# Kernel optimization log

Hardware: AMD Instinct MI355X
Metric: run time of the kernel (lower is better)

## Reference

```python
import jax, jax.numpy as jnp
import numpy as np

HEADS = 16
HEAD_DIM = 64
NEG = 1000000000.0  # additive mask magnitude from source


def setup_inputs() -> dict:
    key = jax.random.key(0)
    ks = jax.random.split(key, 6)
    N, S, D = 4, 2048, 1024
    x = jax.random.normal(ks[0], (N, S, D), dtype=jnp.float32)
    scale = 1.0 / np.sqrt(D)
    wq = jax.random.normal(ks[1], (D, D), dtype=jnp.float32) * scale
    wk = jax.random.normal(ks[2], (D, D), dtype=jnp.float32) * scale
    wv = jax.random.normal(ks[3], (D, D), dtype=jnp.float32) * scale
    wo = jax.random.normal(ks[4], (D, D), dtype=jnp.float32) * scale
    bo = jnp.zeros((D,), dtype=jnp.float32)
    return {"x": x, "wq": wq, "wk": wk, "wv": wv, "wo": wo, "bo": bo}


def reference(x, wq, wk, wv, wo, bo):
    N, S, D = x.shape
    h, d = HEADS, HEAD_DIM
    attn_scale = 1.0 / np.sqrt(d)
    # projections (no bias, qkv_bias=False)
    q = (x @ wq.T).reshape(N, S, h, d).transpose(0, 2, 1, 3)  # N h S d
    k = (x @ wk.T).reshape(N, S, h, d).transpose(0, 2, 1, 3)  # N h S d
    v = (x @ wv.T).reshape(N, S, h, d).transpose(0, 2, 1, 3)  # N h S d
    logits = jnp.einsum('nhsd,nhtd->nhst', q, k) * attn_scale  # N h S S
    scores = jax.nn.softmax(logits, axis=-1)
    # faithful quirk: additive mask applied AFTER softmax
    # triu(ones) - 1 -> 0 on/above diagonal, -1 strictly below
    causal_mask = NEG * (jnp.triu(jnp.ones((S, S), dtype=x.dtype)) - 1.0)
    scores = scores + causal_mask  # broadcasts over N, h
    out = jnp.einsum('nhst,nhtd->nhsd', scores, v)  # N h S d
    out = out.transpose(0, 2, 1, 3).reshape(N, S, h * d)
    return out @ wo.T + bo  # dropout p=0 -> identity
```

## Files before the change

### kernel.cpp

```cpp
#include <hip/hip_runtime.h>

#define AS1 __attribute__((address_space(1)))
#define AS3 __attribute__((address_space(3)))

typedef __bf16 bf16x8 __attribute__((ext_vector_type(8)));
typedef float f32x4 __attribute__((ext_vector_type(4)));

__device__ __forceinline__ unsigned short f2bf(float f) {
  unsigned int u = __float_as_uint(f);
  return (unsigned short)((u + 0x7fffu + ((u >> 16) & 1u)) >> 16);
}

__device__ __forceinline__ void gemm_body(int bx, int by, int bz,
                                          const unsigned short* __restrict__ A,
                                          const unsigned short* __restrict__ B,
                                          float* __restrict__ C,
                                          const float* __restrict__ bias,
                                          int ldC, int K, int kchunk, int planeElems,
                                          unsigned short* lA, unsigned short* lB) {
  int tid = threadIdx.x;
  int w = tid >> 6, lane = tid & 63;
  int r0 = bx * 128, c0 = by * 128;
  int wr = w >> 1, wc = w & 1;
  int ml = lane & 15, q = lane >> 4;
  C += (size_t)bz * planeElems;

  int srow = lane >> 3;
  int scol = 8 * ((lane & 7) ^ srow);
  const unsigned short* gA = A + (size_t)(r0 + 32 * w + srow) * K + scol + (size_t)bz * kchunk;
  const unsigned short* gB = B + (size_t)(c0 + 32 * w + srow) * K + scol + (size_t)bz * kchunk;
  unsigned short* lAp = lA + 32 * w * 64;
  unsigned short* lBp = lB + 32 * w * 64;

  const f32x4 vzero = {0.f, 0.f, 0.f, 0.f};
  f32x4 acc[4][4];
#pragma unroll
  for (int mt = 0; mt < 4; ++mt)
#pragma unroll
    for (int nt = 0; nt < 4; ++nt) acc[mt][nt] = vzero;

  for (int k0 = 0; k0 < kchunk; k0 += 64) {
#pragma unroll
    for (int n = 0; n < 4; ++n) {
      __builtin_amdgcn_global_load_lds((const AS1 void*)(gA + (size_t)8 * n * K + k0),
                                       (AS3 void*)(lAp + n * 512), 16, 0, 0);
      __builtin_amdgcn_global_load_lds((const AS1 void*)(gB + (size_t)8 * n * K + k0),
                                       (AS3 void*)(lBp + n * 512), 16, 0, 0);
    }
    __syncthreads();
#pragma unroll
    for (int h = 0; h < 2; ++h) {
      bf16x8 af[4], bfv[4];
      int kb = 4 * h + q;
#pragma unroll
      for (int mt = 0; mt < 4; ++mt) {
        int R = 64 * wr + 16 * mt + ml;
        af[mt] = *(const bf16x8*)(lA + R * 64 + 8 * (kb ^ (ml & 7)));
      }
#pragma unroll
      for (int nt = 0; nt < 4; ++nt) {
        int R = 64 * wc + 16 * nt + ml;
        bfv[nt] = *(const bf16x8*)(lB + R * 64 + 8 * (kb ^ (ml & 7)));
      }
#pragma unroll
      for (int mt = 0; mt < 4; ++mt)
#pragma unroll
        for (int nt = 0; nt < 4; ++nt)
          acc[mt][nt] = __builtin_amdgcn_mfma_f32_16x16x32_bf16(af[mt], bfv[nt], acc[mt][nt], 0, 0, 0);
    }
    __syncthreads();
  }

#pragma unroll
  for (int nt = 0; nt < 4; ++nt) {
    int col = c0 + 64 * wc + 16 * nt + ml;
    float bv = bias ? bias[col] : 0.f;
#pragma unroll
    for (int mt = 0; mt < 4; ++mt) {
      int rowb = r0 + 64 * wr + 16 * mt + q * 4;
#pragma unroll
      for (int r = 0; r < 4; ++r)
        C[(size_t)(rowb + r) * ldC + col] = acc[mt][nt][r] + bv;
    }
  }
}

__global__ __launch_bounds__(256) void prep_tilesum_k(const float* __restrict__ x,
                                                      const float* __restrict__ wo,
                                                      const float* __restrict__ wv,
                                                      float* __restrict__ T,
                                                      unsigned short* __restrict__ wo_b,
                                                      unsigned short* __restrict__ wvT_b) {
  __shared__ float t[32][33];
  int b = blockIdx.x;
  if (b < 512) {
    int bt = b >> 2;
    int f = (b & 3) * 256 + threadIdx.x;
    const float* p = x + (size_t)bt * 65536 + f;
    float s = 0.f;
#pragma unroll 8
    for (int i = 0; i < 64; ++i) s += p[(size_t)i * 1024];
    T[(size_t)bt * 1024 + f] = s;
  } else if (b < 1536) {
    int i = ((b - 512) * 256 + threadIdx.x) * 4;
    float4 v = *(const float4*)(wo + i);
    ushort4 o;
    o.x = f2bf(v.x); o.y = f2bf(v.y); o.z = f2bf(v.z); o.w = f2bf(v.w);
    *(ushort4*)(wo_b + i) = o;
  } else {
    int bb = b - 1536;
    int bx = (bb & 31) * 32, by = (bb >> 5) * 32;
    int tx = threadIdx.x & 31, ty = threadIdx.x >> 5;
    for (int i = ty; i < 32; i += 8) t[i][tx] = wv[(by + i) * 1024 + bx + tx];
    __syncthreads();
    for (int i = ty; i < 32; i += 8) wvT_b[(bx + i) * 1024 + by + tx] = f2bf(t[tx][i]);
  }
}

__global__ __launch_bounds__(256) void scan_smallgemm_k(const float* __restrict__ x,
                                                        const float* __restrict__ T,
                                                        unsigned short* __restrict__ Xc,
                                                        const unsigned short* __restrict__ wo_b,
                                                        const unsigned short* __restrict__ wvT_b,
                                                        float* __restrict__ Pf) {
  __shared__ unsigned short lA[128 * 64];
  __shared__ unsigned short lB[128 * 64];
  int b = blockIdx.x;
  if (b < 512) {
    int bt = b >> 2;
    int tile = bt & 31, b0 = bt - tile;
    int f = (b & 3) * 256 + threadIdx.x;
    float acc = 0.f;
    for (int t = 0; t < tile; ++t) acc += T[(size_t)(b0 + t) * 1024 + f];
    const float* px = x + (size_t)bt * 65536 + f;
    unsigned short* po = Xc + (size_t)bt * 65536 + f;
#pragma unroll 4
    for (int i = 0; i < 64; ++i) {
      po[(size_t)i * 1024] = f2bf(acc);
      acc += px[(size_t)i * 1024];
    }
  } else {
    int g = b - 512;
    gemm_body(g & 7, (g >> 3) & 7, g >> 6, wo_b, wvT_b, Pf, nullptr,
              1024, 1024, 256, 1 << 20, lA, lB);
  }
}

__global__ __launch_bounds__(256) void reduce_cast_k(const float* __restrict__ P,
                                                     unsigned short* __restrict__ Mp) {
  int i = (blockIdx.x * 256 + threadIdx.x) * 4;
  float4 a = *(const float4*)(P + i);
  float4 b = *(const float4*)(P + (1u << 20) + i);
  float4 c = *(const float4*)(P + (2u << 20) + i);
  float4 d = *(const float4*)(P + (3u << 20) + i);
  ushort4 o;
  o.x = f2bf(-1e9f * (a.x + b.x + c.x + d.x));
  o.y = f2bf(-1e9f * (a.y + b.y + c.y + d.y));
  o.z = f2bf(-1e9f * (a.z + b.z + c.z + d.z));
  o.w = f2bf(-1e9f * (a.w + b.w + c.w + d.w));
  *(ushort4*)(Mp + i) = o;
}

__global__ __launch_bounds__(256) void gemm_big_k(const unsigned short* __restrict__ A,
                                                  const unsigned short* __restrict__ B,
                                                  float* __restrict__ C,
                                                  const float* __restrict__ bias) {
  __shared__ unsigned short lA[128 * 64];
  __shared__ unsigned short lB[128 * 64];
  gemm_body(blockIdx.x, blockIdx.y, 0, A, B, C, bias, 1024, 1024, 1024, 0, lA, lB);
}

extern "C" void kernel_launch(void* const* d_in, const int* in_sizes, int n_in,
                              void* d_out, int out_size, void* d_ws, size_t ws_size,
                              hipStream_t stream) {
  const float* x  = (const float*)d_in[0];
  const float* wv = (const float*)d_in[3];
  const float* wo = (const float*)d_in[4];
  const float* bo = (const float*)d_in[5];
  char* ws = (char*)d_ws;

  unsigned short* wo_b  = (unsigned short*)ws;
  unsigned short* wvT_b = (unsigned short*)(ws + (2u << 20));
  unsigned short* Mp    = (unsigned short*)(ws + (4u << 20));
  float*          Tsum  = (float*)(ws + (6u << 20));
  unsigned short* Xc    = (unsigned short*)(ws + (7u << 20));
  float*          Pf    = (float*)(ws + (23u << 20));

  prep_tilesum_k<<<2560, 256, 0, stream>>>(x, wo, wv, Tsum, wo_b, wvT_b);
  scan_smallgemm_k<<<768, 256, 0, stream>>>(x, Tsum, Xc, wo_b, wvT_b, Pf);
  reduce_cast_k<<<1024, 256, 0, stream>>>(Pf, Mp);
  gemm_big_k<<<dim3(64, 8), 256, 0, stream>>>(Xc, Mp, (float*)d_out, bo);
}
```

Baseline: 146.0 us.

## Fuse tile-sum into scan kernel with flag-based inter-block prefix chaining

The per-tile column sums of x are no longer computed in a separate pass over x. The scan kernel now loads its 64-row tile into registers once, publishes the tile total with a release store and a flag, and spin-waits on the flags of earlier tiles to build its prefix. The goal is to read x only once and avoid holding it in registers across a kernel boundary. In exchange it adds a serial dependency chain across blocks, spin-waits, and a deadlock risk if earlier blocks are not resident, and the 64-float register array raises register pressure.

```diff
diff --git a/kernel.cpp b/kernel.cpp
--- a/kernel.cpp
+++ b/kernel.cpp
@@ -29,8 +29,8 @@
   int scol = 8 * ((lane & 7) ^ srow);
   const unsigned short* gA = A + (size_t)(r0 + 32 * w + srow) * K + scol + (size_t)bz * kchunk;
   const unsigned short* gB = B + (size_t)(c0 + 32 * w + srow) * K + scol + (size_t)bz * kchunk;
-  unsigned short* lAp = lA + 32 * w * 64;
-  unsigned short* lBp = lB + 32 * w * 64;
+  unsigned short* lApw = lA + 32 * w * 64;
+  unsigned short* lBpw = lB + 32 * w * 64;
 
   const f32x4 vzero = {0.f, 0.f, 0.f, 0.f};
   f32x4 acc[4][4];
@@ -43,9 +43,9 @@
 #pragma unroll
     for (int n = 0; n < 4; ++n) {
       __builtin_amdgcn_global_load_lds((const AS1 void*)(gA + (size_t)8 * n * K + k0),
-                                       (AS3 void*)(lAp + n * 512), 16, 0, 0);
+                                       (AS3 void*)(lApw + n * 512), 16, 0, 0);
       __builtin_amdgcn_global_load_lds((const AS1 void*)(gB + (size_t)8 * n * K + k0),
-                                       (AS3 void*)(lBp + n * 512), 16, 0, 0);
+                                       (AS3 void*)(lBpw + n * 512), 16, 0, 0);
     }
     __syncthreads();
 #pragma unroll
@@ -85,63 +85,72 @@
   }
 }
 
-__global__ __launch_bounds__(256) void prep_tilesum_k(const float* __restrict__ x,
-                                                      const float* __restrict__ wo,
-                                                      const float* __restrict__ wv,
-                                                      float* __restrict__ T,
-                                                      unsigned short* __restrict__ wo_b,
-                                                      unsigned short* __restrict__ wvT_b) {
+__global__ __launch_bounds__(256) void prep_k(const float* __restrict__ wo,
+                                              const float* __restrict__ wv,
+                                              unsigned short* __restrict__ wo_b,
+                                              unsigned short* __restrict__ wvT_b,
+                                              int* __restrict__ flags) {
   __shared__ float t[32][33];
   int b = blockIdx.x;
-  if (b < 512) {
-    int bt = b >> 2;
-    int f = (b & 3) * 256 + threadIdx.x;
-    const float* p = x + (size_t)bt * 65536 + f;
-    float s = 0.f;
-#pragma unroll 8
-    for (int i = 0; i < 64; ++i) s += p[(size_t)i * 1024];
-    T[(size_t)bt * 1024 + f] = s;
-  } else if (b < 1536) {
-    int i = ((b - 512) * 256 + threadIdx.x) * 4;
+  if (b < 1024) {
+    int i = (b * 256 + threadIdx.x) * 4;
     float4 v = *(const float4*)(wo + i);
     ushort4 o;
     o.x = f2bf(v.x); o.y = f2bf(v.y); o.z = f2bf(v.z); o.w = f2bf(v.w);
     *(ushort4*)(wo_b + i) = o;
-  } else {
-    int bb = b - 1536;
+  } else if (b < 2048) {
+    int bb = b - 1024;
     int bx = (bb & 31) * 32, by = (bb >> 5) * 32;
     int tx = threadIdx.x & 31, ty = threadIdx.x >> 5;
     for (int i = ty; i < 32; i += 8) t[i][tx] = wv[(by + i) * 1024 + bx + tx];
     __syncthreads();
     for (int i = ty; i < 32; i += 8) wvT_b[(bx + i) * 1024 + by + tx] = f2bf(t[tx][i]);
+  } else {
+    flags[threadIdx.x] = 0;
+    flags[256 + threadIdx.x] = 0;
   }
 }
 
 __global__ __launch_bounds__(256) void scan_smallgemm_k(const float* __restrict__ x,
-                                                        const float* __restrict__ T,
+                                                        float* __restrict__ T,
+                                                        int* __restrict__ flags,
                                                         unsigned short* __restrict__ Xc,
                                                         const unsigned short* __restrict__ wo_b,
                                                         const unsigned short* __restrict__ wvT_b,
                                                         float* __restrict__ Pf) {
   __shared__ unsigned short lA[128 * 64];
   __shared__ unsigned short lB[128 * 64];
-  int b = blockIdx.x;
-  if (b < 512) {
-    int bt = b >> 2;
+  int g = blockIdx.x;
+  if (g < 512) {
+    int bt = g >> 2, fg = g & 3;
     int tile = bt & 31, b0 = bt - tile;
-    int f = (b & 3) * 256 + threadIdx.x;
-    float acc = 0.f;
-    for (int t = 0; t < tile; ++t) acc += T[(size_t)(b0 + t) * 1024 + f];
+    int f = fg * 256 + threadIdx.x;
     const float* px = x + (size_t)bt * 65536 + f;
+    float v[64];
+    float tot = 0.f;
+#pragma unroll
+    for (int i = 0; i < 64; ++i) { v[i] = px[(size_t)i * 1024]; tot += v[i]; }
+    __hip_atomic_store(&T[(size_t)bt * 1024 + f], tot, __ATOMIC_RELEASE,
+                       __HIP_MEMORY_SCOPE_AGENT);
+    __syncthreads();
+    if (threadIdx.x == 0)
+      __hip_atomic_store(&flags[g], 1, __ATOMIC_RELEASE, __HIP_MEMORY_SCOPE_AGENT);
+    float pref = 0.f;
+    for (int t = 0; t < tile; ++t) {
+      int pg = (b0 + t) * 4 + fg;
+      if (threadIdx.x == 0)
+        while (__hip_atomic_load(&flags[pg], __ATOMIC_ACQUIRE,
+                                 __HIP_MEMORY_SCOPE_AGENT) == 0) {}
+      __syncthreads();
+      pref += __hip_atomic_load(&T[(size_t)(b0 + t) * 1024 + f], __ATOMIC_RELAXED,
+                                __HIP_MEMORY_SCOPE_AGENT);
+    }
     unsigned short* po = Xc + (size_t)bt * 65536 + f;
-#pragma unroll 4
-    for (int i = 0; i < 64; ++i) {
-      po[(size_t)i * 1024] = f2bf(acc);
-      acc += px[(size_t)i * 1024];
-    }
+#pragma unroll
+    for (int i = 0; i < 64; ++i) { po[(size_t)i * 1024] = f2bf(pref); pref += v[i]; }
   } else {
-    int g = b - 512;
-    gemm_body(g & 7, (g >> 3) & 7, g >> 6, wo_b, wvT_b, Pf, nullptr,
+    int gg = g - 512;
+    gemm_body(gg & 7, (gg >> 3) & 7, gg >> 6, wo_b, wvT_b, Pf, nullptr,
               1024, 1024, 256, 1 << 20, lA, lB);
   }
 }
@@ -183,11 +192,12 @@
   unsigned short* wvT_b = (unsigned short*)(ws + (2u << 20));
   unsigned short* Mp    = (unsigned short*)(ws + (4u << 20));
   float*          Tsum  = (float*)(ws + (6u << 20));
+  int*            flags = (int*)(ws + (6u << 20) + (1u << 19));
   unsigned short* Xc    = (unsigned short*)(ws + (7u << 20));
   float*          Pf    = (float*)(ws + (23u << 20));
 
-  prep_tilesum_k<<<2560, 256, 0, stream>>>(x, wo, wv, Tsum, wo_b, wvT_b);
-  scan_smallgemm_k<<<768, 256, 0, stream>>>(x, Tsum, Xc, wo_b, wvT_b, Pf);
+  prep_k<<<2049, 256, 0, stream>>>(wo, wv, wo_b, wvT_b, flags);
+  scan_smallgemm_k<<<768, 256, 0, stream>>>(x, Tsum, flags, Xc, wo_b, wvT_b, Pf);
   reduce_cast_k<<<1024, 256, 0, stream>>>(Pf, Mp);
   gemm_big_k<<<dim3(64, 8), 256, 0, stream>>>(Xc, Mp, (float*)d_out, bo);
 }
```

Measured after the change: 247.6 us. 1.7x slower.
